# Kernel tuning notes

Measured on AMD Instinct MI355X. Metric: run time of the kernel, lower is better.

Reference implementation:

```python
import jax, jax.numpy as jnp
import numpy as np

DIM = 1024
HEADS = 16
HEAD_DIM = DIM // HEADS
SCALE = HEAD_DIM ** -0.5
EPS = 1e-5


def layernorm(x, g, b):
    mu = jnp.mean(x, axis=-1, keepdims=True)
    var = jnp.mean((x - mu) ** 2, axis=-1, keepdims=True)
    return (x - mu) * jax.lax.rsqrt(var + EPS) * g + b


def setup_inputs() -> dict:
    key = jax.random.key(0)
    ks = jax.random.split(key, 12)
    B, N = 2, 2048
    s = DIM ** -0.5
    return {
        "q": jax.random.normal(ks[0], (B, N, DIM), jnp.float32),
        "k": jax.random.normal(ks[1], (B, N, DIM), jnp.float32),
        "v": jax.random.normal(ks[2], (B, N, DIM), jnp.float32),
        "gq": jnp.ones((DIM,), jnp.float32), "bq_ln": jnp.zeros((DIM,), jnp.float32),
        "gk": jnp.ones((DIM,), jnp.float32), "bk_ln": jnp.zeros((DIM,), jnp.float32),
        "gv": jnp.ones((DIM,), jnp.float32), "bv_ln": jnp.zeros((DIM,), jnp.float32),
        "Wq": jax.random.normal(ks[3], (DIM, DIM), jnp.float32) * s,
        "bq": jnp.zeros((DIM,), jnp.float32),
        "Wk": jax.random.normal(ks[4], (DIM, DIM), jnp.float32) * s,
        "bk": jnp.zeros((DIM,), jnp.float32),
        "Wv": jax.random.normal(ks[5], (DIM, DIM), jnp.float32) * s,
        "bv": jnp.zeros((DIM,), jnp.float32),
        "Wp": jax.random.normal(ks[6], (DIM, DIM), jnp.float32) * s,
        "bp": jnp.zeros((DIM,), jnp.float32),
    }


def reference(q, k, v, gq, bq_ln, gk, bk_ln, gv, bv_ln, Wq, bq, Wk, bk, Wv, bv, Wp, bp):
    B, Nq, C = q.shape
    Nk, Nv = k.shape[1], v.shape[1]
    qn = layernorm(q, gq, bq_ln)
    kn = layernorm(k, gk, bk_ln)
    vn = layernorm(v, gv, bv_ln)
    # project and split heads -> [B, H, N, hd]
    qh = (qn @ Wq + bq).reshape(B, Nq, HEADS, HEAD_DIM).transpose(0, 2, 1, 3)
    kh = (kn @ Wk + bk).reshape(B, Nk, HEADS, HEAD_DIM).transpose(0, 2, 1, 3)
    vh = (vn @ Wv + bv).reshape(B, Nv, HEADS, HEAD_DIM).transpose(0, 2, 1, 3)
    attn = jnp.einsum("bhqd,bhkd->bhqk", qh, kh) * SCALE
    attn = jax.nn.softmax(attn, axis=-1)
    out = jnp.einsum("bhqk,bhkd->bhqd", attn, vh)
    out = out.transpose(0, 2, 1, 3).reshape(B, Nq, C)
    out = out @ Wp + bp
    return (out, kh, vh)
```

## Files before the change

kernel.cpp:

```cpp
#include <hip/hip_runtime.h>
#include <cstdint>

#define DIMC 1024
#define NSEQ 2048
#define BATCH 2
#define HEADS 16
#define HD 64
#define MROWS (BATCH * NSEQ)

typedef unsigned short u16;
typedef unsigned int u32;
typedef __attribute__((ext_vector_type(8))) short bf16x8;
typedef __attribute__((ext_vector_type(4))) float f32x4;

#if __has_builtin(__builtin_amdgcn_exp2f)
#define EXP2(x) __builtin_amdgcn_exp2f(x)
#else
#define EXP2(x) exp2f(x)
#endif

__device__ __forceinline__ u16 f2bf(float f) {
  union { float f; u32 u; } v; v.f = f;
  u32 u = v.u;
  return (u16)((u + 0x7fffu + ((u >> 16) & 1u)) >> 16);
}
__device__ __forceinline__ u32 pack_rne(float a, float b) {
  return (u32)f2bf(a) | ((u32)f2bf(b) << 16);
}
__device__ __forceinline__ u32 pack_trunc(float a, float b) {
  union { float f; u32 u; } x, y; x.f = a; y.f = b;
  return (x.u >> 16) | (y.u & 0xffff0000u);
}
__device__ __forceinline__ void gload_lds16(const void* g, void* l) {
  __builtin_amdgcn_global_load_lds((const __attribute__((address_space(1))) void*)g,
                                   (__attribute__((address_space(3))) void*)l, 16, 0, 0);
}

__global__ __launch_bounds__(256)
void prep(const float* __restrict__ q, const float* __restrict__ k,
          const float* __restrict__ v,
          const float* __restrict__ gq, const float* __restrict__ bq,
          const float* __restrict__ gk, const float* __restrict__ bk,
          const float* __restrict__ gv, const float* __restrict__ bv,
          const float* __restrict__ w0, const float* __restrict__ w1,
          const float* __restrict__ w2, const float* __restrict__ w3,
          u16* __restrict__ xn, u16* __restrict__ wtout) {
  __shared__ float rs[4], rs2[4];
  __shared__ float tile[32][33];
  int tid = threadIdx.x;
  if (blockIdx.x < 3 * MROWS) {
    int rowid = blockIdx.x;
    int tensor = rowid >> 12;
    int r = rowid & 4095;
    const float *src, *g, *b;
    if (tensor == 0)      { src = q; g = gq; b = bq; }
    else if (tensor == 1) { src = k; g = gk; b = bk; }
    else                  { src = v; g = gv; b = bv; }
    src += (size_t)r * DIMC;
    u16* dst = xn + (size_t)tensor * MROWS * DIMC + (size_t)r * DIMC;
    float4 x = ((const float4*)src)[tid];
    float s  = x.x + x.y + x.z + x.w;
    float s2 = x.x*x.x + x.y*x.y + x.z*x.z + x.w*x.w;
    #pragma unroll
    for (int m = 1; m < 64; m <<= 1) { s += __shfl_xor(s, m); s2 += __shfl_xor(s2, m); }
    int wave = tid >> 6, lane = tid & 63;
    if (lane == 0) { rs[wave] = s; rs2[wave] = s2; }
    __syncthreads();
    s  = rs[0] + rs[1] + rs[2] + rs[3];
    s2 = rs2[0] + rs2[1] + rs2[2] + rs2[3];
    float mu  = s * (1.0f / DIMC);
    float var = s2 * (1.0f / DIMC) - mu * mu;
    float inv = rsqrtf(var + 1e-5f);
    float4 gg = ((const float4*)g)[tid];
    float4 bb = ((const float4*)b)[tid];
    uint2 o;
    o.x = pack_rne((x.x - mu) * inv * gg.x + bb.x, (x.y - mu) * inv * gg.y + bb.y);
    o.y = pack_rne((x.z - mu) * inv * gg.z + bb.z, (x.w - mu) * inv * gg.w + bb.w);
    ((uint2*)dst)[tid] = o;
  } else {
    int blk = blockIdx.x - 3 * MROWS;
    int widx = blk >> 10, t = blk & 1023;
    int ti = t >> 5, tj = t & 31;
    const float* W = (widx == 0) ? w0 : (widx == 1) ? w1 : (widx == 2) ? w2 : w3;
    u16* O = wtout + (size_t)widx * DIMC * DIMC;
    int tx = tid & 31, ty = tid >> 5;
    #pragma unroll
    for (int rr = 0; rr < 32; rr += 8)
      tile[ty + rr][tx] = W[(size_t)(ti * 32 + ty + rr) * DIMC + tj * 32 + tx];
    __syncthreads();
    #pragma unroll
    for (int rr = 0; rr < 32; rr += 8)
      O[(size_t)(tj * 32 + ty + rr) * DIMC + ti * 32 + tx] = f2bf(tile[tx][ty + rr]);
  }
}

__global__ __launch_bounds__(256)
void qkv_gemm(const u16* __restrict__ xn, const u16* __restrict__ wt,
              const float* __restrict__ bq, const float* __restrict__ bk,
              const float* __restrict__ bv,
              float* __restrict__ out, u16* __restrict__ qh,
              u16* __restrict__ khb, u16* __restrict__ vtb) {
  __shared__ u16 smem[128 * 136];
  u16* As = smem;
  u16* Bs = smem + 4096;
  u16* Ls = smem;
  const int z = blockIdx.z;
  const u16* A  = xn + (size_t)z * MROWS * DIMC;
  const u16* Bt = wt + (size_t)z * DIMC * DIMC;
  const float* bias = (z == 0) ? bq : (z == 1) ? bk : bv;
  const int bm = blockIdx.x, bn = blockIdx.y;
  const int tid = threadIdx.x;
  const int wave = tid >> 6, lane = tid & 63;
  const int wm = (wave & 1) * 64, wn = (wave >> 1) * 64;
  const int row = lane & 15, quad = lane >> 4;
  const float QSCL = 0.18033688011112042f;
  f32x4 acc[4][4] = {};
  for (int k0 = 0; k0 < DIMC; k0 += 32) {
    #pragma unroll
    for (int c = 0; c < 2; ++c) {
      int e = c * 2048 + tid * 8;
      int rr = e >> 5, col = e & 31;
      gload_lds16(&A[(size_t)(bm * 128 + rr) * DIMC + k0 + col], &As[e]);
      gload_lds16(&Bt[(size_t)(bn * 128 + rr) * DIMC + k0 + col], &Bs[e]);
    }
    __syncthreads();
    bf16x8 a[4], b[4];
    #pragma unroll
    for (int i = 0; i < 4; ++i)
      a[i] = *(const bf16x8*)(&As[(wm + i * 16 + row) * 32 + quad * 8]);
    #pragma unroll
    for (int j = 0; j < 4; ++j)
      b[j] = *(const bf16x8*)(&Bs[(wn + j * 16 + row) * 32 + quad * 8]);
    #pragma unroll
    for (int i = 0; i < 4; ++i)
      #pragma unroll
      for (int j = 0; j < 4; ++j)
        acc[i][j] = __builtin_amdgcn_mfma_f32_16x16x32_bf16(a[i], b[j], acc[i][j], 0, 0, 0);
    __syncthreads();
  }
  #pragma unroll
  for (int i = 0; i < 4; ++i) {
    #pragma unroll
    for (int j = 0; j < 4; ++j) {
      float val[4];
      #pragma unroll
      for (int r = 0; r < 4; ++r) {
        int m = bm * 128 + wm + i * 16 + quad * 4 + r;
        int c = bn * 128 + wn + j * 16 + row;
        val[r] = acc[i][j][r] + bias[c];
        int b_ = m >> 11, n = m & 2047, h = c >> 6, d = c & 63;
        int bh = b_ * HEADS + h;
        size_t hidx = ((size_t)bh * NSEQ + n) * HD + d;
        if (z == 0) {
          qh[hidx] = f2bf(val[r] * QSCL);
        } else {
          out[(size_t)z * MROWS * DIMC + hidx] = val[r];
          if (z == 1) khb[hidx] = f2bf(val[r]);
        }
      }
      if (z == 2) {
        int ct = wn + j * 16 + row;
        int mt = wm + i * 16 + quad * 4;
        u32* L = (u32*)(&Ls[ct * 136 + mt]);
        L[0] = pack_rne(val[0], val[1]);
        L[1] = pack_rne(val[2], val[3]);
      }
    }
  }
  if (z == 2) {
    __syncthreads();
    int b_ = (bm * 128) >> 11;
    int nbase = (bm * 128) & 2047;
    #pragma unroll
    for (int it = 0; it < 8; ++it) {
      int idx = it * 256 + tid;
      int ct = idx >> 4, ch = idx & 15;
      uint4 y = *(const uint4*)(&Ls[ct * 136 + ch * 8]);
      int c = bn * 128 + ct;
      int h = c >> 6, d = c & 63;
      size_t rowb = ((size_t)(b_ * HEADS + h) * HD + d) * NSEQ;
      int K0 = nbase + ch * 8;
      int d1 = (K0 & ~31) + ((K0 & 8) ? 16 : 0) + ((K0 & 16) ? 4 : 0);
      uint2 lo; lo.x = y.x; lo.y = y.y;
      uint2 hi; hi.x = y.z; hi.y = y.w;
      *(uint2*)(&vtb[rowb + d1])     = lo;
      *(uint2*)(&vtb[rowb + d1 + 8]) = hi;
    }
  }
}

__global__ __launch_bounds__(256)
void out_gemm(const u16* __restrict__ A, const u16* __restrict__ Bt,
              const float* __restrict__ bias, float* __restrict__ outf) {
  __shared__ u16 As[64 * 32];
  __shared__ u16 Bs[128 * 32];
  const int bm = blockIdx.x, bn = blockIdx.y;
  const int tid = threadIdx.x;
  const int wave = tid >> 6, lane = tid & 63;
  const int wm = (wave & 1) * 32, wn = (wave >> 1) * 64;
  const int row = lane & 15, quad = lane >> 4;
  f32x4 acc[2][4] = {};
  for (int k0 = 0; k0 < DIMC; k0 += 32) {
    {
      int e = tid * 8;
      int rr = e >> 5, col = e & 31;
      gload_lds16(&A[(size_t)(bm * 64 + rr) * DIMC + k0 + col], &As[e]);
    }
    #pragma unroll
    for (int c = 0; c < 2; ++c) {
      int e = c * 2048 + tid * 8;
      int rr = e >> 5, col = e & 31;
      gload_lds16(&Bt[(size_t)(bn * 128 + rr) * DIMC + k0 + col], &Bs[e]);
    }
    __syncthreads();
    bf16x8 a[2], b[4];
    #pragma unroll
    for (int i = 0; i < 2; ++i)
      a[i] = *(const bf16x8*)(&As[(wm + i * 16 + row) * 32 + quad * 8]);
    #pragma unroll
    for (int j = 0; j < 4; ++j)
      b[j] = *(const bf16x8*)(&Bs[(wn + j * 16 + row) * 32 + quad * 8]);
    #pragma unroll
    for (int i = 0; i < 2; ++i)
      #pragma unroll
      for (int j = 0; j < 4; ++j)
        acc[i][j] = __builtin_amdgcn_mfma_f32_16x16x32_bf16(a[i], b[j], acc[i][j], 0, 0, 0);
    __syncthreads();
  }
  #pragma unroll
  for (int i = 0; i < 2; ++i)
    #pragma unroll
    for (int j = 0; j < 4; ++j)
      #pragma unroll
      for (int r = 0; r < 4; ++r) {
        int m = bm * 64 + wm + i * 16 + quad * 4 + r;
        int c = bn * 128 + wn + j * 16 + row;
        outf[(size_t)m * DIMC + c] = acc[i][j][r] + bias[c];
      }
}

__global__ __launch_bounds__(256)
void attn_fused(const u16* __restrict__ qh, const u16* __restrict__ kh,
                const u16* __restrict__ vt, u16* __restrict__ ao) {
  __shared__ u16 Ks[2][64 * 64];
  __shared__ u16 Vs[2][64 * 64];
  const int flat = blockIdx.x;
  const int bh = (flat & 7) * 4 + ((flat >> 3) & 3);
  const int qtile = flat >> 5;
  const int b = bh >> 4, h = bh & 15;
  const int tid = threadIdx.x;
  const int wave = tid >> 6, lane = tid & 63;
  const int qi = lane & 15, quad = lane >> 4;
  const int sw = qi & 7;
  const size_t base = (size_t)bh * NSEQ * HD;
  bf16x8 qf[2][2];
  #pragma unroll
  for (int qt = 0; qt < 2; ++qt) {
    int qrow = qtile * 128 + wave * 32 + qt * 16 + qi;
    #pragma unroll
    for (int dh = 0; dh < 2; ++dh)
      qf[qt][dh] = *(const bf16x8*)(&qh[base + (size_t)qrow * HD + dh * 32 + quad * 8]);
  }
  #pragma unroll
  for (int c = 0; c < 2; ++c) {
    int p = c * 256 + tid;
    int rk = p >> 3, ck = p & 7;
    gload_lds16(&kh[base + (size_t)rk * HD + (ck ^ (rk & 7)) * 8], &Ks[0][p * 8]);
    gload_lds16(&vt[base + (size_t)rk * NSEQ + (ck ^ (rk & 7)) * 8], &Vs[0][p * 8]);
  }
  __syncthreads();
  float li0 = 0.f, li1 = 0.f;
  f32x4 oacc[2][4] = {};
  for (int t = 0; t < NSEQ / 64; ++t) {
    const int cur = t & 1;
    if (t < NSEQ / 64 - 1) {
      #pragma unroll
      for (int c = 0; c < 2; ++c) {
        int p = c * 256 + tid;
        int rk = p >> 3, ck = p & 7;
        gload_lds16(&kh[base + (size_t)((t + 1) * 64 + rk) * HD + (ck ^ (rk & 7)) * 8],
                    &Ks[cur ^ 1][p * 8]);
        gload_lds16(&vt[base + (size_t)rk * NSEQ + (t + 1) * 64 + (ck ^ (rk & 7)) * 8],
                    &Vs[cur ^ 1][p * 8]);
      }
    }
    const u16* Kb = &Ks[cur][0];
    const u16* Vb = &Vs[cur][0];
    #pragma unroll
    for (int kc = 0; kc < 2; ++kc) {
      const u16* kr0 = &Kb[((kc * 2) * 16 + qi) * 64];
      const u16* kr1 = &Kb[((kc * 2 + 1) * 16 + qi) * 64];
      bf16x8 ka0 = *(const bf16x8*)(&kr0[(quad ^ sw) * 8]);
      bf16x8 ka1 = *(const bf16x8*)(&kr0[((4 + quad) ^ sw) * 8]);
      bf16x8 kb0 = *(const bf16x8*)(&kr1[(quad ^ sw) * 8]);
      bf16x8 kb1 = *(const bf16x8*)(&kr1[((4 + quad) ^ sw) * 8]);
      f32x4 s00 = {}, s01 = {}, s10 = {}, s11 = {};
      __builtin_amdgcn_s_setprio(1);
      s00 = __builtin_amdgcn_mfma_f32_16x16x32_bf16(ka0, qf[0][0], s00, 0, 0, 0);
      s00 = __builtin_amdgcn_mfma_f32_16x16x32_bf16(ka1, qf[0][1], s00, 0, 0, 0);
      s01 = __builtin_amdgcn_mfma_f32_16x16x32_bf16(kb0, qf[0][0], s01, 0, 0, 0);
      s01 = __builtin_amdgcn_mfma_f32_16x16x32_bf16(kb1, qf[0][1], s01, 0, 0, 0);
      s10 = __builtin_amdgcn_mfma_f32_16x16x32_bf16(ka0, qf[1][0], s10, 0, 0, 0);
      s10 = __builtin_amdgcn_mfma_f32_16x16x32_bf16(ka1, qf[1][1], s10, 0, 0, 0);
      s11 = __builtin_amdgcn_mfma_f32_16x16x32_bf16(kb0, qf[1][0], s11, 0, 0, 0);
      s11 = __builtin_amdgcn_mfma_f32_16x16x32_bf16(kb1, qf[1][1], s11, 0, 0, 0);
      __builtin_amdgcn_s_setprio(0);
      float a0 = EXP2(s00[0]), a1 = EXP2(s00[1]), a2 = EXP2(s00[2]), a3 = EXP2(s00[3]);
      float a4 = EXP2(s01[0]), a5 = EXP2(s01[1]), a6 = EXP2(s01[2]), a7 = EXP2(s01[3]);
      float b0 = EXP2(s10[0]), b1 = EXP2(s10[1]), b2 = EXP2(s10[2]), b3 = EXP2(s10[3]);
      float b4 = EXP2(s11[0]), b5 = EXP2(s11[1]), b6 = EXP2(s11[2]), b7 = EXP2(s11[3]);
      li0 += ((a0 + a1) + (a2 + a3)) + ((a4 + a5) + (a6 + a7));
      li1 += ((b0 + b1) + (b2 + b3)) + ((b4 + b5) + (b6 + b7));
      union { bf16x8 v; u32 u[4]; } pu0, pu1;
      pu0.u[0] = pack_trunc(a0, a1); pu0.u[1] = pack_trunc(a2, a3);
      pu0.u[2] = pack_trunc(a4, a5); pu0.u[3] = pack_trunc(a6, a7);
      pu1.u[0] = pack_trunc(b0, b1); pu1.u[1] = pack_trunc(b2, b3);
      pu1.u[2] = pack_trunc(b4, b5); pu1.u[3] = pack_trunc(b6, b7);
      __builtin_amdgcn_s_setprio(1);
      #pragma unroll
      for (int dt = 0; dt < 4; ++dt) {
        bf16x8 vf = *(const bf16x8*)(&Vb[(dt * 16 + qi) * 64 + ((kc * 4 + quad) ^ sw) * 8]);
        oacc[0][dt] = __builtin_amdgcn_mfma_f32_16x16x32_bf16(vf, pu0.v, oacc[0][dt], 0, 0, 0);
        oacc[1][dt] = __builtin_amdgcn_mfma_f32_16x16x32_bf16(vf, pu1.v, oacc[1][dt], 0, 0, 0);
      }
      __builtin_amdgcn_s_setprio(0);
    }
    __syncthreads();
  }
  li0 += __shfl_xor(li0, 16); li0 += __shfl_xor(li0, 32);
  li1 += __shfl_xor(li1, 16); li1 += __shfl_xor(li1, 32);
  #pragma unroll
  for (int qt = 0; qt < 2; ++qt) {
    float inv = 1.0f / (qt == 0 ? li0 : li1);
    int token = b * NSEQ + qtile * 128 + wave * 32 + qt * 16 + qi;
    #pragma unroll
    for (int dt = 0; dt < 4; ++dt) {
      int col = h * 64 + dt * 16 + quad * 4;
      *(u32*)(&ao[(size_t)token * DIMC + col]) =
          pack_rne(oacc[qt][dt][0] * inv, oacc[qt][dt][1] * inv);
      *(u32*)(&ao[(size_t)token * DIMC + col + 2]) =
          pack_rne(oacc[qt][dt][2] * inv, oacc[qt][dt][3] * inv);
    }
  }
}

extern "C" void kernel_launch(void* const* d_in, const int* in_sizes, int n_in,
                              void* d_out, int out_size, void* d_ws, size_t ws_size,
                              hipStream_t stream) {
  const float* q    = (const float*)d_in[0];
  const float* k    = (const float*)d_in[1];
  const float* v    = (const float*)d_in[2];
  const float* gq   = (const float*)d_in[3];
  const float* bqln = (const float*)d_in[4];
  const float* gk   = (const float*)d_in[5];
  const float* bkln = (const float*)d_in[6];
  const float* gv   = (const float*)d_in[7];
  const float* bvln = (const float*)d_in[8];
  const float* Wq   = (const float*)d_in[9];
  const float* bq   = (const float*)d_in[10];
  const float* Wk   = (const float*)d_in[11];
  const float* bk   = (const float*)d_in[12];
  const float* Wv   = (const float*)d_in[13];
  const float* bv   = (const float*)d_in[14];
  const float* Wp   = (const float*)d_in[15];
  const float* bp   = (const float*)d_in[16];
  float* out = (float*)d_out;

  char* ws = (char*)d_ws;
  u16* xn  = (u16*)(ws);
  u16* wt  = (u16*)(ws + (size_t)25165824);
  u16* qh  = (u16*)(ws + (size_t)33554432);
  u16* khb = (u16*)(ws + (size_t)41943040);
  u16* ao  = (u16*)(ws + (size_t)50331648);
  u16* vtb = (u16*)d_out;

  const size_t WEL = (size_t)DIMC * DIMC;

  prep<<<3 * MROWS + 4096, 256, 0, stream>>>(q, k, v, gq, bqln, gk, bkln, gv, bvln,
                                             Wq, Wk, Wv, Wp, xn, wt);
  qkv_gemm<<<dim3(MROWS / 128, DIMC / 128, 3), 256, 0, stream>>>(
      xn, wt, bq, bk, bv, out, qh, khb, vtb);
  attn_fused<<<dim3((NSEQ / 128) * BATCH * HEADS), 256, 0, stream>>>(qh, khb, vtb, ao);
  out_gemm<<<dim3(MROWS / 64, DIMC / 128), 256, 0, stream>>>(ao, wt + 3 * WEL, bp, out);
}
```

Before: 241.3 us.

## Split attention over two key halves with atomic accumulation and a combine pass

The attention kernel now splits the key sequence into two halves. Each block processes 16 key tiles and atomically adds its unnormalized output and row sums into fp32 workspace buffers. A new combine kernel then normalizes the result and writes bf16 for the output projection. Doubling the block count is meant to fill more CUs, at the cost of a memset, fp32 atomic traffic and an extra kernel launch. Separately, layernorm prep now handles one row per wavefront, four rows per block, which removes the shared-memory reduction and the block barrier.

```diff
diff --git a/kernel.cpp b/kernel.cpp
--- a/kernel.cpp
+++ b/kernel.cpp
@@ -45,11 +45,11 @@
           const float* __restrict__ w0, const float* __restrict__ w1,
           const float* __restrict__ w2, const float* __restrict__ w3,
           u16* __restrict__ xn, u16* __restrict__ wtout) {
-  __shared__ float rs[4], rs2[4];
   __shared__ float tile[32][33];
   int tid = threadIdx.x;
-  if (blockIdx.x < 3 * MROWS) {
-    int rowid = blockIdx.x;
+  if (blockIdx.x < 3 * MROWS / 4) {
+    int wave = tid >> 6, lane = tid & 63;
+    int rowid = blockIdx.x * 4 + wave;
     int tensor = rowid >> 12;
     int r = rowid & 4095;
     const float *src, *g, *b;
@@ -58,27 +58,30 @@
     else                  { src = v; g = gv; b = bv; }
     src += (size_t)r * DIMC;
     u16* dst = xn + (size_t)tensor * MROWS * DIMC + (size_t)r * DIMC;
-    float4 x = ((const float4*)src)[tid];
-    float s  = x.x + x.y + x.z + x.w;
-    float s2 = x.x*x.x + x.y*x.y + x.z*x.z + x.w*x.w;
+    float4 x[4];
+    float s = 0.f, s2 = 0.f;
+    #pragma unroll
+    for (int j = 0; j < 4; ++j) {
+      x[j] = ((const float4*)src)[j * 64 + lane];
+      s  += x[j].x + x[j].y + x[j].z + x[j].w;
+      s2 += x[j].x*x[j].x + x[j].y*x[j].y + x[j].z*x[j].z + x[j].w*x[j].w;
+    }
     #pragma unroll
     for (int m = 1; m < 64; m <<= 1) { s += __shfl_xor(s, m); s2 += __shfl_xor(s2, m); }
-    int wave = tid >> 6, lane = tid & 63;
-    if (lane == 0) { rs[wave] = s; rs2[wave] = s2; }
-    __syncthreads();
-    s  = rs[0] + rs[1] + rs[2] + rs[3];
-    s2 = rs2[0] + rs2[1] + rs2[2] + rs2[3];
     float mu  = s * (1.0f / DIMC);
     float var = s2 * (1.0f / DIMC) - mu * mu;
     float inv = rsqrtf(var + 1e-5f);
-    float4 gg = ((const float4*)g)[tid];
-    float4 bb = ((const float4*)b)[tid];
-    uint2 o;
-    o.x = pack_rne((x.x - mu) * inv * gg.x + bb.x, (x.y - mu) * inv * gg.y + bb.y);
-    o.y = pack_rne((x.z - mu) * inv * gg.z + bb.z, (x.w - mu) * inv * gg.w + bb.w);
-    ((uint2*)dst)[tid] = o;
+    #pragma unroll
+    for (int j = 0; j < 4; ++j) {
+      float4 gg = ((const float4*)g)[j * 64 + lane];
+      float4 bb = ((const float4*)b)[j * 64 + lane];
+      uint2 o;
+      o.x = pack_rne((x[j].x - mu) * inv * gg.x + bb.x, (x[j].y - mu) * inv * gg.y + bb.y);
+      o.y = pack_rne((x[j].z - mu) * inv * gg.z + bb.z, (x[j].w - mu) * inv * gg.w + bb.w);
+      ((uint2*)dst)[j * 64 + lane] = o;
+    }
   } else {
-    int blk = blockIdx.x - 3 * MROWS;
+    int blk = blockIdx.x - 3 * MROWS / 4;
     int widx = blk >> 10, t = blk & 1023;
     int ti = t >> 5, tj = t & 31;
     const float* W = (widx == 0) ? w0 : (widx == 1) ? w1 : (widx == 2) ? w2 : w3;
@@ -241,18 +244,21 @@
 
 __global__ __launch_bounds__(256)
 void attn_fused(const u16* __restrict__ qh, const u16* __restrict__ kh,
-                const u16* __restrict__ vt, u16* __restrict__ ao) {
+                const u16* __restrict__ vt,
+                float* __restrict__ Oacc, float* __restrict__ Li) {
   __shared__ u16 Ks[2][64 * 64];
   __shared__ u16 Vs[2][64 * 64];
   const int flat = blockIdx.x;
   const int bh = (flat & 7) * 4 + ((flat >> 3) & 3);
-  const int qtile = flat >> 5;
+  const int qtile = (flat >> 5) & 15;
+  const int ks = flat >> 9;
   const int b = bh >> 4, h = bh & 15;
   const int tid = threadIdx.x;
   const int wave = tid >> 6, lane = tid & 63;
   const int qi = lane & 15, quad = lane >> 4;
   const int sw = qi & 7;
   const size_t base = (size_t)bh * NSEQ * HD;
+  const int t0 = ks * 16;
   bf16x8 qf[2][2];
   #pragma unroll
   for (int qt = 0; qt < 2; ++qt) {
@@ -265,15 +271,16 @@
   for (int c = 0; c < 2; ++c) {
     int p = c * 256 + tid;
     int rk = p >> 3, ck = p & 7;
-    gload_lds16(&kh[base + (size_t)rk * HD + (ck ^ (rk & 7)) * 8], &Ks[0][p * 8]);
-    gload_lds16(&vt[base + (size_t)rk * NSEQ + (ck ^ (rk & 7)) * 8], &Vs[0][p * 8]);
+    gload_lds16(&kh[base + (size_t)(t0 * 64 + rk) * HD + (ck ^ (rk & 7)) * 8], &Ks[0][p * 8]);
+    gload_lds16(&vt[base + (size_t)rk * NSEQ + t0 * 64 + (ck ^ (rk & 7)) * 8], &Vs[0][p * 8]);
   }
   __syncthreads();
   float li0 = 0.f, li1 = 0.f;
   f32x4 oacc[2][4] = {};
-  for (int t = 0; t < NSEQ / 64; ++t) {
-    const int cur = t & 1;
-    if (t < NSEQ / 64 - 1) {
+  for (int tt = 0; tt < 16; ++tt) {
+    const int t = t0 + tt;
+    const int cur = tt & 1;
+    if (tt < 15) {
       #pragma unroll
       for (int c = 0; c < 2; ++c) {
         int p = c * 256 + tid;
@@ -331,17 +338,36 @@
   li1 += __shfl_xor(li1, 16); li1 += __shfl_xor(li1, 32);
   #pragma unroll
   for (int qt = 0; qt < 2; ++qt) {
-    float inv = 1.0f / (qt == 0 ? li0 : li1);
     int token = b * NSEQ + qtile * 128 + wave * 32 + qt * 16 + qi;
+    if (quad == 0) atomicAdd(&Li[(size_t)token * HEADS + h], qt == 0 ? li0 : li1);
     #pragma unroll
     for (int dt = 0; dt < 4; ++dt) {
-      int col = h * 64 + dt * 16 + quad * 4;
-      *(u32*)(&ao[(size_t)token * DIMC + col]) =
-          pack_rne(oacc[qt][dt][0] * inv, oacc[qt][dt][1] * inv);
-      *(u32*)(&ao[(size_t)token * DIMC + col + 2]) =
-          pack_rne(oacc[qt][dt][2] * inv, oacc[qt][dt][3] * inv);
-    }
-  }
+      float* dst = &Oacc[(size_t)token * DIMC + h * 64 + dt * 16 + quad * 4];
+      atomicAdd(dst + 0, oacc[qt][dt][0]);
+      atomicAdd(dst + 1, oacc[qt][dt][1]);
+      atomicAdd(dst + 2, oacc[qt][dt][2]);
+      atomicAdd(dst + 3, oacc[qt][dt][3]);
+    }
+  }
+}
+
+__global__ __launch_bounds__(256)
+void combine(const float* __restrict__ Oacc, const float* __restrict__ Li,
+             u16* __restrict__ ao) {
+  int i = blockIdx.x * 256 + threadIdx.x;
+  size_t e0 = (size_t)i * 16;
+  int token = (int)(e0 >> 10);
+  int c0 = (int)(e0 & 1023);
+  float inv = 1.0f / Li[(size_t)token * HEADS + (c0 >> 6)];
+  const float4* src = (const float4*)(Oacc + e0);
+  float4 x0 = src[0], x1 = src[1], x2 = src[2], x3 = src[3];
+  uint4 r0, r1;
+  r0.x = pack_rne(x0.x * inv, x0.y * inv); r0.y = pack_rne(x0.z * inv, x0.w * inv);
+  r0.z = pack_rne(x1.x * inv, x1.y * inv); r0.w = pack_rne(x1.z * inv, x1.w * inv);
+  r1.x = pack_rne(x2.x * inv, x2.y * inv); r1.y = pack_rne(x2.z * inv, x2.w * inv);
+  r1.z = pack_rne(x3.x * inv, x3.y * inv); r1.w = pack_rne(x3.z * inv, x3.w * inv);
+  *(uint4*)(&ao[e0]) = r0;
+  *(uint4*)(&ao[e0 + 8]) = r1;
 }
 
 extern "C" void kernel_launch(void* const* d_in, const int* in_sizes, int n_in,
@@ -372,14 +398,19 @@
   u16* qh  = (u16*)(ws + (size_t)33554432);
   u16* khb = (u16*)(ws + (size_t)41943040);
   u16* ao  = (u16*)(ws + (size_t)50331648);
+  float* Oacc = (float*)ws;
+  float* Li   = (float*)(ws + (size_t)16777216);
   u16* vtb = (u16*)d_out;
 
   const size_t WEL = (size_t)DIMC * DIMC;
 
-  prep<<<3 * MROWS + 4096, 256, 0, stream>>>(q, k, v, gq, bqln, gk, bkln, gv, bvln,
-                                             Wq, Wk, Wv, Wp, xn, wt);
+  prep<<<3 * MROWS / 4 + 4096, 256, 0, stream>>>(q, k, v, gq, bqln, gk, bkln, gv, bvln,
+                                                 Wq, Wk, Wv, Wp, xn, wt);
   qkv_gemm<<<dim3(MROWS / 128, DIMC / 128, 3), 256, 0, stream>>>(
       xn, wt, bq, bk, bv, out, qh, khb, vtb);
-  attn_fused<<<dim3((NSEQ / 128) * BATCH * HEADS), 256, 0, stream>>>(qh, khb, vtb, ao);
+  hipMemsetAsync(ws, 0, (size_t)16777216 + 262144, stream);
+  attn_fused<<<dim3((NSEQ / 128) * BATCH * HEADS * 2), 256, 0, stream>>>(
+      qh, khb, vtb, Oacc, Li);
+  combine<<<dim3(MROWS * DIMC / 16 / 256), 256, 0, stream>>>(Oacc, Li, ao);
   out_gemm<<<dim3(MROWS / 64, DIMC / 128), 256, 0, stream>>>(ao, wt + 3 * WEL, bp, out);
 }
```

Measured after the change: 348.5 us. 44.4% more time.
